# Kernel optimization log

Hardware: AMD Instinct MI355X
Metric: run time of the kernel (lower is better)

Reference implementation:

```python
import jax, jax.numpy as jnp
import numpy as np

N, E = 50000, 800000
IN_DIM, OUT_DIM, EDGE_DIM = 128, 128, 6
LN_EPS = 1e-5


def setup_inputs() -> dict:
    key = jax.random.key(0)
    ks = jax.random.split(key, 9)
    w = lambda k, sh: (jax.random.normal(k, sh, jnp.float32) * 0.05)
    return {
        "x": jax.random.normal(ks[0], (N, IN_DIM), jnp.float32),
        "edge_attr": jax.random.normal(ks[1], (E, EDGE_DIM), jnp.float32),
        "Wn": w(ks[2], (IN_DIM, OUT_DIM)),
        "bn": jnp.zeros((OUT_DIM,), jnp.float32),
        "We": w(ks[3], (EDGE_DIM, OUT_DIM)),
        "be": jnp.zeros((OUT_DIM,), jnp.float32),
        "Wm": w(ks[4], (2 * OUT_DIM, OUT_DIM)),
        "bm": jnp.zeros((OUT_DIM,), jnp.float32),
        "gamma": jnp.ones((OUT_DIM,), jnp.float32),
        "beta": jnp.zeros((OUT_DIM,), jnp.float32),
        "edge_index": jax.random.randint(ks[5], (2, E), 0, N, jnp.int32),
    }


def reference(x, edge_attr, Wn, bn, We, be, Wm, bm, gamma, beta, edge_index):
    row, col = edge_index[0], edge_index[1]
    x_t = x @ Wn + bn                                  # [N, D]
    e_t = edge_attr @ We + be                          # [E, D]
    msgs = jnp.concatenate([x_t[col], e_t], axis=-1)   # gather + concat [E, 2D]
    msgs = jax.nn.relu(msgs @ Wm + bm)                 # [E, D]
    agg = jax.ops.segment_sum(msgs, row, num_segments=N)            # scatter_add
    deg = jax.ops.segment_sum(jnp.ones((E,), jnp.float32), row, num_segments=N)
    out = agg / jnp.clip(deg, 1.0)[:, None] + x_t      # mean-normalize + residual
    mu = out.mean(axis=-1, keepdims=True)
    var = out.var(axis=-1, keepdims=True)
    return (out - mu) * jax.lax.rsqrt(var + LN_EPS) * gamma + beta
```

## Files before the change

### kernel.cpp

```cpp
#include <hip/hip_runtime.h>
#include <hip/hip_bf16.h>

#define D 128
#define EDGE_DIM 6
#define LN_EPS 1e-5f
#define HIST_BLOCKS 2048
#define BINE 2048
#define CB 256
#define NB2 196

typedef __attribute__((ext_vector_type(8))) short short8;
typedef __attribute__((ext_vector_type(4))) float f32x4;
typedef __attribute__((ext_vector_type(2))) float f32x2;

static __device__ __forceinline__ float bf_lo(unsigned u) { return __uint_as_float(u << 16); }
static __device__ __forceinline__ float bf_hi(unsigned u) { return __uint_as_float(u & 0xffff0000u); }
static __device__ __forceinline__ unsigned short f2bf(float f) {
    __hip_bfloat16 h = __float2bfloat16(f);
    return *reinterpret_cast<unsigned short*>(&h);
}
static __device__ __forceinline__ unsigned f2fp8(float f) {
    unsigned u;
    asm("v_cvt_pk_fp8_f32 %0, %1, %2" : "=v"(u) : "v"(f), "v"(0.0f));
    return u & 0xffu;
}
static __device__ __forceinline__ unsigned f2fp8pair(float a, float b) {
    unsigned u;
    asm("v_cvt_pk_fp8_f32 %0, %1, %2" : "=v"(u) : "v"(a), "v"(b));
    return u & 0xffffu;
}
static __device__ __forceinline__ f32x2 cvt2_fp8v(unsigned w) {
    f32x2 r;
    asm("v_cvt_pk_f32_fp8 %0, %1" : "=v"(r) : "v"(w));
    return r;
}
static __device__ __forceinline__ f32x2 cvt2_fp8s(unsigned w) {
    f32x2 r;
    asm("v_cvt_pk_f32_fp8 %0, %1" : "=v"(r) : "s"(w));
    return r;
}

__global__ __launch_bounds__(128)
void setup_all(const float* __restrict__ Wn, const float* __restrict__ bn,
               const float* __restrict__ We, const float* __restrict__ be,
               const float* __restrict__ Wm, const float* __restrict__ bm,
               const int* __restrict__ ei, int E,
               float* __restrict__ Wnm, float* __restrict__ bnm,
               float* __restrict__ Wc, float* __restrict__ bc,
               int* __restrict__ cnt) {
    const int b = blockIdx.x;
    const int d = threadIdx.x;
    if (b < 128) {
        float acc = 0.f;
#pragma unroll 8
        for (int j = 0; j < D; ++j)
            acc = fmaf(Wn[b * D + j], Wm[j * D + d], acc);
        Wnm[b * D + d] = acc;
    } else if (b == 128) {
        float acc = 0.f;
#pragma unroll 8
        for (int j = 0; j < D; ++j)
            acc = fmaf(bn[j], Wm[j * D + d], acc);
        bnm[d] = acc;
    } else if (b < 135) {
        const int k = b - 129;
        float acc = 0.f;
#pragma unroll 8
        for (int j = 0; j < D; ++j)
            acc = fmaf(We[k * D + j], Wm[(D + j) * D + d], acc);
        Wc[k * D + d] = acc;
    } else if (b == 135) {
        float acc = bm[d];
#pragma unroll 8
        for (int j = 0; j < D; ++j)
            acc = fmaf(be[j], Wm[(D + j) * D + d], acc);
        bc[d] = acc;
    } else {
        for (int i = (b - 136) * 128 + d; i < E; i += HIST_BLOCKS * 128)
            atomicAdd(&cnt[ei[i]], 1);
    }
}

__global__ __launch_bounds__(1024)
void scan_pack(const int* __restrict__ cnt, int* __restrict__ start,
               int* __restrict__ cur2, int* __restrict__ cursor, int n, int nscan,
               const float* __restrict__ Wn, const float* __restrict__ Wnm,
               unsigned short* __restrict__ Wb) {
    const int tid = threadIdx.x;
    if ((int)blockIdx.x >= nscan) {
        const int idx = ((int)blockIdx.x - nscan) * 1024 + tid;
        if (idx < 4096) {
            const int lane = idx & 63;
            const int s = (idx >> 6) & 3;
            const int ct = (idx >> 8) & 7;
            const int mat = idx >> 11;
            const float* W = mat ? Wnm : Wn;
            const int col = ct * 16 + (lane & 15);
            const int k0 = (lane >> 4) * 8 + 32 * s;
            short8 v;
#pragma unroll
            for (int j = 0; j < 8; ++j)
                v[j] = (short)f2bf(W[(size_t)(k0 + j) * D + col]);
            *reinterpret_cast<short8*>(Wb + (size_t)idx * 8) = v;
        }
        return;
    }
    __shared__ int wsum[16];
    __shared__ int sbase;
    const int lane = tid & 63, wid = tid >> 6;
    const int i = blockIdx.x * 1024 + tid;
    const int v = (i < n) ? cnt[i] : 0;
    int x = v;
#pragma unroll
    for (int off = 1; off < 64; off <<= 1) {
        int t = __shfl_up(x, off);
        if (lane >= off) x += t;
    }
    if (lane == 63) wsum[wid] = x;
    __syncthreads();
    if (wid == 0) {
        int w = (lane < 16) ? wsum[lane] : 0;
#pragma unroll
        for (int off = 1; off < 16; off <<= 1) {
            int t = __shfl_up(w, off);
            if (lane >= off) w += t;
        }
        if (lane < 16) wsum[lane] = w;
    }
    __syncthreads();
    const int total = wsum[15];
    if (tid == 0) sbase = atomicAdd(cursor, total);
    __syncthreads();
    const int woff = (wid > 0) ? wsum[wid - 1] : 0;
    if (i < n) {
        const int sv = sbase + woff + x - v;
        start[i] = sv;
        if ((i & (CB - 1)) == 0) cur2[i >> 8] = sv;
    }
}

__global__ __launch_bounds__(256)
void scat_gemm(const int* __restrict__ ei, int E, const float* __restrict__ ea,
               int* __restrict__ cur2, uint2* __restrict__ tmp,
               unsigned char* __restrict__ tmpR, int nbin,
               const float* __restrict__ x, const unsigned short* __restrict__ Wb,
               const float* __restrict__ bn, const float* __restrict__ bnm,
               unsigned short* __restrict__ xtb, unsigned char* __restrict__ hb,
               int nrows) {
    __shared__ unsigned short sP[BINE * 3];
    __shared__ int hist[NB2];
    __shared__ int cbase[NB2];
    const int tid = threadIdx.x;
    if ((int)blockIdx.x < nbin) {
        const int base = blockIdx.x * BINE;
        const int nrec = min(BINE, E - base);
        if (tid < NB2) hist[tid] = 0;
        const float2* ea2 = reinterpret_cast<const float2*>(ea);
        for (int i = tid; i < nrec * 3; i += 256) {
            float2 p = ea2[(size_t)base * 3 + i];
            sP[i] = (unsigned short)f2fp8pair(p.x, p.y);
        }
        int rows[8], cols[8];
#pragma unroll
        for (int it = 0; it < 8; ++it) {
            const int e = base + it * 256 + tid;
            const bool val = e < E;
            rows[it] = val ? ei[e] : -1;
            cols[it] = val ? ei[E + e] : 0;
        }
        __syncthreads();
#pragma unroll
        for (int it = 0; it < 8; ++it)
            if (rows[it] >= 0) atomicAdd(&hist[rows[it] >> 8], 1);
        __syncthreads();
        if (tid < NB2) {
            const int hv = hist[tid];
            cbase[tid] = hv ? atomicAdd(&cur2[tid], hv) : 0;
            hist[tid] = 0;
        }
        __syncthreads();
#pragma unroll
        for (int it = 0; it < 8; ++it)
            if (rows[it] >= 0) {
                const int bkt = rows[it] >> 8;
                const int lp = atomicAdd(&hist[bkt], 1);
                const int pos = cbase[bkt] + lp;
                const int le = (it * 256 + tid) * 3;
                const unsigned w0 = (unsigned)cols[it] | ((unsigned)sP[le] << 16);
                const unsigned w1 = (unsigned)sP[le + 1] | ((unsigned)sP[le + 2] << 16);
                tmp[pos] = make_uint2(w0, w1);
                tmpR[pos] = (unsigned char)(rows[it] & (CB - 1));
            }
        return;
    }
    const int ntile = (nrows + 15) / 16;
    const int lane = tid & 63;
    const int wid = tid >> 6;
    const int t = ((int)blockIdx.x - nbin) * 4 + wid;
    if (t >= ntile) return;
    const int row16 = lane & 15;
    const int kgrp = lane >> 4;

    float biasA[8], biasB[8];
#pragma unroll
    for (int ct = 0; ct < 8; ++ct) {
        biasA[ct] = bn[ct * 16 + row16];
        biasB[ct] = bnm[ct * 16 + row16];
    }
    const int ra = t * 16 + row16;
    const bool rv = ra < nrows;
    short8 a[4];
#pragma unroll
    for (int s = 0; s < 4; ++s) {
        const float* xp = x + (size_t)ra * D + kgrp * 8 + 32 * s;
        float4 u0 = rv ? *reinterpret_cast<const float4*>(xp)
                       : make_float4(0.f, 0.f, 0.f, 0.f);
        float4 u1 = rv ? *reinterpret_cast<const float4*>(xp + 4)
                       : make_float4(0.f, 0.f, 0.f, 0.f);
        a[s][0] = (short)f2bf(u0.x); a[s][1] = (short)f2bf(u0.y);
        a[s][2] = (short)f2bf(u0.z); a[s][3] = (short)f2bf(u0.w);
        a[s][4] = (short)f2bf(u1.x); a[s][5] = (short)f2bf(u1.y);
        a[s][6] = (short)f2bf(u1.z); a[s][7] = (short)f2bf(u1.w);
    }
    const int rw0 = t * 16 + kgrp * 4;
#pragma unroll
    for (int mat = 0; mat < 2; ++mat) {
#pragma unroll
        for (int ct = 0; ct < 8; ++ct) {
            f32x4 acc = {0.f, 0.f, 0.f, 0.f};
#pragma unroll
            for (int s = 0; s < 4; ++s) {
                short8 bfr = *reinterpret_cast<const short8*>(
                    Wb + (size_t)((((mat * 8 + ct) * 4 + s) * 64 + lane)) * 8);
                acc = __builtin_amdgcn_mfma_f32_16x16x32_bf16(a[s], bfr, acc, 0, 0, 0);
            }
            const float bsc = mat ? biasB[ct] : biasA[ct];
            const int dcol = ct * 16 + row16;
#pragma unroll
            for (int j = 0; j < 4; ++j) {
                const int r = rw0 + j;
                if (r < nrows) {
                    if (mat == 0)
                        xtb[(size_t)r * D + dcol] = f2bf(acc[j] + bsc);
                    else
                        hb[(size_t)r * D + dcol] = (unsigned char)f2fp8(acc[j] + bsc);
                }
            }
        }
    }
}

__global__ __launch_bounds__(512)
void resort(const uint2* __restrict__ tmp, const unsigned char* __restrict__ tmpR,
            const int* __restrict__ start, const int* __restrict__ cnt,
            uint2* __restrict__ rec, int nnode) {
    __shared__ uint2 sRec[2048];
    __shared__ unsigned char sRow[2048];
    __shared__ int ncur[CB];
    const int tid = threadIdx.x;
    const int b = blockIdx.x;
    const int nodes0 = b * CB;
    const int nn = min(CB, nnode - nodes0);
    if (tid < CB) ncur[tid] = (tid < nn) ? start[nodes0 + tid] : 0;
    __syncthreads();
    const int s0 = start[nodes0];
    const int lastn = nodes0 + nn - 1;
    const int count = start[lastn] + cnt[lastn] - s0;
    for (int base = 0; base < count; base += 2048) {
        const int m = min(2048, count - base);
        for (int i = tid; i < m; i += 512) {
            sRec[i] = tmp[(size_t)(s0 + base) + i];
            sRow[i] = tmpR[(size_t)(s0 + base) + i];
        }
        __syncthreads();
        for (int i = tid; i < m; i += 512) {
            const int rl = sRow[i];
            const int pos = atomicAdd(&ncur[rl], 1);
            rec[pos] = sRec[i];
        }
        __syncthreads();
    }
}

__global__ __launch_bounds__(256)
void aggregate_ln(const unsigned char* __restrict__ h8,
                  const int* __restrict__ start, const int* __restrict__ cnt,
                  const uint2* __restrict__ rec,
                  const float* __restrict__ Wc, const float* __restrict__ bc,
                  const unsigned* __restrict__ xtb,
                  const float* __restrict__ gamma, const float* __restrict__ beta,
                  float* __restrict__ out, int nnode) {
    const int lane = threadIdx.x & 63;
    const int wid = threadIdx.x >> 6;

    f32x2 wc[EDGE_DIM];
#pragma unroll
    for (int k = 0; k < EDGE_DIM; ++k)
        wc[k] = reinterpret_cast<const f32x2*>(Wc)[k * 64 + lane];
    const f32x2 bc2 = reinterpret_cast<const f32x2*>(bc)[lane];
    const f32x2 g = reinterpret_cast<const f32x2*>(gamma)[lane];
    const f32x2 bb = reinterpret_cast<const f32x2*>(beta)[lane];

    for (int n = blockIdx.x * 4 + wid; n < nnode; n += gridDim.x * 4) {
        const int s = start[n];
        const int c = cnt[n];
        const unsigned xu = xtb[(unsigned)(n * 64 + lane)];
        f32x2 axy = {0.f, 0.f};
        for (int ibase = 0; ibase < c; ibase += 64) {
            const int m = min(64, c - ibase);
            uint2 rc = make_uint2(0, 0);
            if (lane < m) rc = rec[(size_t)(s + ibase) + lane];
            auto LDH = [&](int j) -> unsigned {
                const int jc = min(j, m - 1);
                const unsigned colj =
                    (unsigned)__builtin_amdgcn_readlane((int)rc.x, jc) & 0xffffu;
                const unsigned short* hrow =
                    reinterpret_cast<const unsigned short*>(h8 + ((size_t)colj << 7));
                return hrow[lane];
            };
            auto COMP = [&](int j, unsigned hv) {
                const unsigned w0 = (unsigned)__builtin_amdgcn_readlane((int)rc.x, j);
                const unsigned w1 = (unsigned)__builtin_amdgcn_readlane((int)rc.y, j);
                const f32x2 e01 = cvt2_fp8s(w0 >> 16);
                const f32x2 e23 = cvt2_fp8s(w1 & 0xffffu);
                const f32x2 e45 = cvt2_fp8s(w1 >> 16);
                const f32x2 hx = cvt2_fp8v(hv);
                f32x2 mA, mB;
                asm("v_pk_add_f32 %0, %1, %2" : "=v"(mA) : "v"(bc2), "v"(hx));
                asm("v_pk_mul_f32 %0, %1, %2 op_sel:[1,0] op_sel_hi:[1,1]"
                    : "=v"(mB) : "v"(e01), "v"(wc[1]));
                asm("v_pk_fma_f32 %0, %1, %2, %0 op_sel:[0,0,0] op_sel_hi:[0,1,1]"
                    : "+v"(mA) : "v"(e01), "v"(wc[0]));
                asm("v_pk_fma_f32 %0, %1, %2, %0 op_sel:[1,0,0] op_sel_hi:[1,1,1]"
                    : "+v"(mB) : "v"(e23), "v"(wc[3]));
                asm("v_pk_fma_f32 %0, %1, %2, %0 op_sel:[0,0,0] op_sel_hi:[0,1,1]"
                    : "+v"(mA) : "v"(e23), "v"(wc[2]));
                asm("v_pk_fma_f32 %0, %1, %2, %0 op_sel:[1,0,0] op_sel_hi:[1,1,1]"
                    : "+v"(mB) : "v"(e45), "v"(wc[5]));
                asm("v_pk_fma_f32 %0, %1, %2, %0 op_sel:[0,0,0] op_sel_hi:[0,1,1]"
                    : "+v"(mA) : "v"(e45), "v"(wc[4]));
                asm("v_pk_add_f32 %0, %0, %1" : "+v"(mA) : "v"(mB));
                axy[0] += fmaxf(mA[0], 0.f);
                axy[1] += fmaxf(mA[1], 0.f);
            };
            unsigned h0 = LDH(0), h1 = LDH(1), h2 = LDH(2), h3 = LDH(3),
                     h4 = LDH(4), h5 = LDH(5), h6 = LDH(6), h7 = LDH(7);
            int i = 0;
            for (; i + 8 <= m; i += 8) {
                COMP(i + 0, h0); h0 = LDH(i + 8);
                COMP(i + 1, h1); h1 = LDH(i + 9);
                COMP(i + 2, h2); h2 = LDH(i + 10);
                COMP(i + 3, h3); h3 = LDH(i + 11);
                COMP(i + 4, h4); h4 = LDH(i + 12);
                COMP(i + 5, h5); h5 = LDH(i + 13);
                COMP(i + 6, h6); h6 = LDH(i + 14);
                COMP(i + 7, h7); h7 = LDH(i + 15);
            }
            if (i + 0 < m) COMP(i + 0, h0);
            if (i + 1 < m) COMP(i + 1, h1);
            if (i + 2 < m) COMP(i + 2, h2);
            if (i + 3 < m) COMP(i + 3, h3);
            if (i + 4 < m) COMP(i + 4, h4);
            if (i + 5 < m) COMP(i + 5, h5);
            if (i + 6 < m) COMP(i + 6, h6);
        }
        const float inv = 1.0f / fmaxf((float)c, 1.0f);
        float o0 = fmaf(axy[0], inv, bf_lo(xu));
        float o1 = fmaf(axy[1], inv, bf_hi(xu));
        float s1 = o0 + o1, s2 = o0 * o0 + o1 * o1;
#pragma unroll
        for (int off = 32; off; off >>= 1) {
            s1 += __shfl_xor(s1, off);
            s2 += __shfl_xor(s2, off);
        }
        const float mean = s1 * (1.0f / D);
        const float var = s2 * (1.0f / D) - mean * mean;
        const float rstd = rsqrtf(var + LN_EPS);
        float2 r;
        r.x = (o0 - mean) * rstd * g[0] + bb[0];
        r.y = (o1 - mean) * rstd * g[1] + bb[1];
        reinterpret_cast<float2*>(out)[(size_t)n * 64 + lane] = r;
    }
}

extern "C" void kernel_launch(void* const* d_in, const int* in_sizes, int n_in,
                              void* d_out, int out_size, void* d_ws, size_t ws_size,
                              hipStream_t stream) {
    const float* x     = (const float*)d_in[0];
    const float* eattr = (const float*)d_in[1];
    const float* Wn    = (const float*)d_in[2];
    const float* bn    = (const float*)d_in[3];
    const float* We    = (const float*)d_in[4];
    const float* be    = (const float*)d_in[5];
    const float* Wm    = (const float*)d_in[6];
    const float* bm    = (const float*)d_in[7];
    const float* gamma = (const float*)d_in[8];
    const float* beta  = (const float*)d_in[9];
    const int*   ei    = (const int*)d_in[10];

    const int N = in_sizes[0] / D;
    const int E = in_sizes[10] / 2;

    char* ws = (char*)d_ws;
    unsigned short* xtb = (unsigned short*)ws; ws += (size_t)N * D * 2;
    unsigned char*  hb  = (unsigned char*)ws;  ws += (size_t)N * D;
    int* ints = (int*)ws;                      ws += (size_t)(N + 4) * 4;
    int* cnt = ints;
    int* cursor = ints + N;
    int* cur2   = (int*)ws;                    ws += (size_t)(NB2 + 1) * 4;
    int* startv = (int*)ws;                    ws += (size_t)N * 4;
    uint2* rec  = (uint2*)ws;                  ws += (size_t)E * 8;
    float* Wnm  = (float*)ws;                  ws += (size_t)D * D * 4;
    float* bnm  = (float*)ws;                  ws += (size_t)D * 4;
    float* Wc   = (float*)ws;                  ws += (size_t)EDGE_DIM * D * 4;
    float* bcv  = (float*)ws;                  ws += (size_t)D * 4;
    unsigned short* Wb = (unsigned short*)ws;  ws += (size_t)4096 * 8 * 2;

    uint2* tmp = (uint2*)d_out;
    unsigned char* tmpR = (unsigned char*)d_out + (size_t)E * 8;

    const int nscan = (N + 1023) / 1024;
    const int nbin = (E + BINE - 1) / BINE;
    const int ntile = (N + 15) / 16;

    hipMemsetAsync(ints, 0, (size_t)(N + 4) * 4, stream);

    setup_all<<<136 + HIST_BLOCKS, 128, 0, stream>>>(Wn, bn, We, be, Wm, bm, ei, E,
                                                     Wnm, bnm, Wc, bcv, cnt);
    scan_pack<<<nscan + 4, 1024, 0, stream>>>(cnt, startv, cur2, cursor, N, nscan,
                                              Wn, Wnm, Wb);
    scat_gemm<<<nbin + (ntile + 3) / 4, 256, 0, stream>>>(ei, E, eattr, cur2, tmp, tmpR,
                                                          nbin, x, Wb, bn, bnm, xtb, hb, N);
    resort<<<NB2, 512, 0, stream>>>(tmp, tmpR, startv, cnt, rec, N);
    aggregate_ln<<<(N + 3) / 4, 256, 0, stream>>>(hb, startv, cnt, rec,
                                                  Wc, bcv, (const unsigned*)xtb,
                                                  gamma, beta, (float*)d_out, N);
}
```

Baseline: 149.8 us.

## Split wavefront into two half-waves each processing a different edge per step

The aggregation kernel now has each half of the 64-lane wavefront handle a different edge, with each lane covering four output features instead of two. Each lane loads a 4-byte fp8 row slice, so one gather instruction fetches two full 128-feature rows and the number of sequential edge iterations is halved. The halves are combined with a cross-half shuffle before the layernorm, and only the lower half writes the output as float4. The cost is more readlanes and selects per step, per-lane edge-feature conversions (vector instead of scalar), a masked accumulate for odd counts, and higher register pressure.

```diff
diff --git a/kernel.cpp b/kernel.cpp
--- a/kernel.cpp
+++ b/kernel.cpp
@@ -32,11 +32,6 @@
 static __device__ __forceinline__ f32x2 cvt2_fp8v(unsigned w) {
     f32x2 r;
     asm("v_cvt_pk_f32_fp8 %0, %1" : "=v"(r) : "v"(w));
-    return r;
-}
-static __device__ __forceinline__ f32x2 cvt2_fp8s(unsigned w) {
-    f32x2 r;
-    asm("v_cvt_pk_f32_fp8 %0, %1" : "=v"(r) : "s"(w));
     return r;
 }
 
@@ -292,94 +287,131 @@
                   float* __restrict__ out, int nnode) {
     const int lane = threadIdx.x & 63;
     const int wid = threadIdx.x >> 6;
-
-    f32x2 wc[EDGE_DIM];
-#pragma unroll
-    for (int k = 0; k < EDGE_DIM; ++k)
-        wc[k] = reinterpret_cast<const f32x2*>(Wc)[k * 64 + lane];
-    const f32x2 bc2 = reinterpret_cast<const f32x2*>(bc)[lane];
-    const f32x2 g = reinterpret_cast<const f32x2*>(gamma)[lane];
-    const f32x2 bb = reinterpret_cast<const f32x2*>(beta)[lane];
+    const int l5 = lane & 31;
+    const int half = lane >> 5;
+
+    f32x2 wcA[EDGE_DIM], wcB[EDGE_DIM];
+#pragma unroll
+    for (int k = 0; k < EDGE_DIM; ++k) {
+        wcA[k] = reinterpret_cast<const f32x2*>(Wc + k * D)[2 * l5];
+        wcB[k] = reinterpret_cast<const f32x2*>(Wc + k * D)[2 * l5 + 1];
+    }
+    const f32x2 bcA = reinterpret_cast<const f32x2*>(bc)[2 * l5];
+    const f32x2 bcB = reinterpret_cast<const f32x2*>(bc)[2 * l5 + 1];
 
     for (int n = blockIdx.x * 4 + wid; n < nnode; n += gridDim.x * 4) {
         const int s = start[n];
         const int c = cnt[n];
-        const unsigned xu = xtb[(unsigned)(n * 64 + lane)];
-        f32x2 axy = {0.f, 0.f};
+        f32x2 accA = {0.f, 0.f}, accB = {0.f, 0.f};
         for (int ibase = 0; ibase < c; ibase += 64) {
             const int m = min(64, c - ibase);
+            const int mq = (m + 1) >> 1;
             uint2 rc = make_uint2(0, 0);
             if (lane < m) rc = rec[(size_t)(s + ibase) + lane];
-            auto LDH = [&](int j) -> unsigned {
-                const int jc = min(j, m - 1);
-                const unsigned colj =
-                    (unsigned)__builtin_amdgcn_readlane((int)rc.x, jc) & 0xffffu;
-                const unsigned short* hrow =
-                    reinterpret_cast<const unsigned short*>(h8 + ((size_t)colj << 7));
-                return hrow[lane];
+            auto LDP = [&](int t) -> unsigned {
+                const int jA = 2 * t;
+                const int jB = min(2 * t + 1, m - 1);
+                const unsigned cA = (unsigned)__builtin_amdgcn_readlane((int)rc.x, jA) & 0xffffu;
+                const unsigned cB = (unsigned)__builtin_amdgcn_readlane((int)rc.x, jB) & 0xffffu;
+                const unsigned col = half ? cB : cA;
+                return *reinterpret_cast<const unsigned*>(
+                    h8 + ((size_t)col << 7) + 4 * l5);
             };
-            auto COMP = [&](int j, unsigned hv) {
-                const unsigned w0 = (unsigned)__builtin_amdgcn_readlane((int)rc.x, j);
-                const unsigned w1 = (unsigned)__builtin_amdgcn_readlane((int)rc.y, j);
-                const f32x2 e01 = cvt2_fp8s(w0 >> 16);
-                const f32x2 e23 = cvt2_fp8s(w1 & 0xffffu);
-                const f32x2 e45 = cvt2_fp8s(w1 >> 16);
-                const f32x2 hx = cvt2_fp8v(hv);
-                f32x2 mA, mB;
-                asm("v_pk_add_f32 %0, %1, %2" : "=v"(mA) : "v"(bc2), "v"(hx));
+            auto PCOMP = [&](int t, unsigned hv) {
+                const int jA = 2 * t;
+                const int jBr = min(2 * t + 1, m - 1);
+                const unsigned w0A = (unsigned)__builtin_amdgcn_readlane((int)rc.x, jA);
+                const unsigned w0B = (unsigned)__builtin_amdgcn_readlane((int)rc.x, jBr);
+                const unsigned w1A = (unsigned)__builtin_amdgcn_readlane((int)rc.y, jA);
+                const unsigned w1B = (unsigned)__builtin_amdgcn_readlane((int)rc.y, jBr);
+                const unsigned w0 = half ? w0B : w0A;
+                const unsigned w1 = half ? w1B : w1A;
+                const f32x2 e01 = cvt2_fp8v(w0 >> 16);
+                const f32x2 e23 = cvt2_fp8v(w1 & 0xffffu);
+                const f32x2 e45 = cvt2_fp8v(w1 >> 16);
+                const f32x2 h01 = cvt2_fp8v(hv);
+                const f32x2 h23 = cvt2_fp8v(hv >> 16);
+                f32x2 mA, mB, nA, nB;
+                asm("v_pk_add_f32 %0, %1, %2" : "=v"(mA) : "v"(bcA), "v"(h01));
+                asm("v_pk_add_f32 %0, %1, %2" : "=v"(nA) : "v"(bcB), "v"(h23));
                 asm("v_pk_mul_f32 %0, %1, %2 op_sel:[1,0] op_sel_hi:[1,1]"
-                    : "=v"(mB) : "v"(e01), "v"(wc[1]));
-                asm("v_pk_fma_f32 %0, %1, %2, %0 op_sel:[0,0,0] op_sel_hi:[0,1,1]"
-                    : "+v"(mA) : "v"(e01), "v"(wc[0]));
+                    : "=v"(mB) : "v"(e01), "v"(wcA[1]));
+                asm("v_pk_mul_f32 %0, %1, %2 op_sel:[1,0] op_sel_hi:[1,1]"
+                    : "=v"(nB) : "v"(e01), "v"(wcB[1]));
+                asm("v_pk_fma_f32 %0, %1, %2, %0 op_sel:[0,0,0] op_sel_hi:[0,1,1]"
+                    : "+v"(mA) : "v"(e01), "v"(wcA[0]));
+                asm("v_pk_fma_f32 %0, %1, %2, %0 op_sel:[0,0,0] op_sel_hi:[0,1,1]"
+                    : "+v"(nA) : "v"(e01), "v"(wcB[0]));
                 asm("v_pk_fma_f32 %0, %1, %2, %0 op_sel:[1,0,0] op_sel_hi:[1,1,1]"
-                    : "+v"(mB) : "v"(e23), "v"(wc[3]));
-                asm("v_pk_fma_f32 %0, %1, %2, %0 op_sel:[0,0,0] op_sel_hi:[0,1,1]"
-                    : "+v"(mA) : "v"(e23), "v"(wc[2]));
+                    : "+v"(mB) : "v"(e23), "v"(wcA[3]));
                 asm("v_pk_fma_f32 %0, %1, %2, %0 op_sel:[1,0,0] op_sel_hi:[1,1,1]"
-                    : "+v"(mB) : "v"(e45), "v"(wc[5]));
-                asm("v_pk_fma_f32 %0, %1, %2, %0 op_sel:[0,0,0] op_sel_hi:[0,1,1]"
-                    : "+v"(mA) : "v"(e45), "v"(wc[4]));
+                    : "+v"(nB) : "v"(e23), "v"(wcB[3]));
+                asm("v_pk_fma_f32 %0, %1, %2, %0 op_sel:[0,0,0] op_sel_hi:[0,1,1]"
+                    : "+v"(mA) : "v"(e23), "v"(wcA[2]));
+                asm("v_pk_fma_f32 %0, %1, %2, %0 op_sel:[0,0,0] op_sel_hi:[0,1,1]"
+                    : "+v"(nA) : "v"(e23), "v"(wcB[2]));
+                asm("v_pk_fma_f32 %0, %1, %2, %0 op_sel:[1,0,0] op_sel_hi:[1,1,1]"
+                    : "+v"(mB) : "v"(e45), "v"(wcA[5]));
+                asm("v_pk_fma_f32 %0, %1, %2, %0 op_sel:[1,0,0] op_sel_hi:[1,1,1]"
+                    : "+v"(nB) : "v"(e45), "v"(wcB[5]));
+                asm("v_pk_fma_f32 %0, %1, %2, %0 op_sel:[0,0,0] op_sel_hi:[0,1,1]"
+                    : "+v"(mA) : "v"(e45), "v"(wcA[4]));
+                asm("v_pk_fma_f32 %0, %1, %2, %0 op_sel:[0,0,0] op_sel_hi:[0,1,1]"
+                    : "+v"(nA) : "v"(e45), "v"(wcB[4]));
                 asm("v_pk_add_f32 %0, %0, %1" : "+v"(mA) : "v"(mB));
-                axy[0] += fmaxf(mA[0], 0.f);
-                axy[1] += fmaxf(mA[1], 0.f);
+                asm("v_pk_add_f32 %0, %0, %1" : "+v"(nA) : "v"(nB));
+                const float keep = (half == 0 || 2 * t + 1 < m) ? 1.0f : 0.0f;
+                accA[0] = fmaf(keep, fmaxf(mA[0], 0.f), accA[0]);
+                accA[1] = fmaf(keep, fmaxf(mA[1], 0.f), accA[1]);
+                accB[0] = fmaf(keep, fmaxf(nA[0], 0.f), accB[0]);
+                accB[1] = fmaf(keep, fmaxf(nA[1], 0.f), accB[1]);
             };
-            unsigned h0 = LDH(0), h1 = LDH(1), h2 = LDH(2), h3 = LDH(3),
-                     h4 = LDH(4), h5 = LDH(5), h6 = LDH(6), h7 = LDH(7);
-            int i = 0;
-            for (; i + 8 <= m; i += 8) {
-                COMP(i + 0, h0); h0 = LDH(i + 8);
-                COMP(i + 1, h1); h1 = LDH(i + 9);
-                COMP(i + 2, h2); h2 = LDH(i + 10);
-                COMP(i + 3, h3); h3 = LDH(i + 11);
-                COMP(i + 4, h4); h4 = LDH(i + 12);
-                COMP(i + 5, h5); h5 = LDH(i + 13);
-                COMP(i + 6, h6); h6 = LDH(i + 14);
-                COMP(i + 7, h7); h7 = LDH(i + 15);
+            unsigned h0 = LDP(0), h1 = 0, h2 = 0, h3 = 0;
+            if (1 < mq) h1 = LDP(1);
+            if (2 < mq) h2 = LDP(2);
+            if (3 < mq) h3 = LDP(3);
+            for (int q = 0; q < 32; q += 4) {
+                if (q >= mq) break;
+                { PCOMP(q + 0, h0); if (q + 4 < mq) h0 = LDP(q + 4); }
+                if (q + 1 < mq) { PCOMP(q + 1, h1); if (q + 5 < mq) h1 = LDP(q + 5); }
+                if (q + 2 < mq) { PCOMP(q + 2, h2); if (q + 6 < mq) h2 = LDP(q + 6); }
+                if (q + 3 < mq) { PCOMP(q + 3, h3); if (q + 7 < mq) h3 = LDP(q + 7); }
             }
-            if (i + 0 < m) COMP(i + 0, h0);
-            if (i + 1 < m) COMP(i + 1, h1);
-            if (i + 2 < m) COMP(i + 2, h2);
-            if (i + 3 < m) COMP(i + 3, h3);
-            if (i + 4 < m) COMP(i + 4, h4);
-            if (i + 5 < m) COMP(i + 5, h5);
-            if (i + 6 < m) COMP(i + 6, h6);
-        }
+        }
+        accA[0] += __shfl_xor(accA[0], 32);
+        accA[1] += __shfl_xor(accA[1], 32);
+        accB[0] += __shfl_xor(accB[0], 32);
+        accB[1] += __shfl_xor(accB[1], 32);
+
         const float inv = 1.0f / fmaxf((float)c, 1.0f);
-        float o0 = fmaf(axy[0], inv, bf_lo(xu));
-        float o1 = fmaf(axy[1], inv, bf_hi(xu));
-        float s1 = o0 + o1, s2 = o0 * o0 + o1 * o1;
-#pragma unroll
-        for (int off = 32; off; off >>= 1) {
+        const uint2 xq = reinterpret_cast<const uint2*>(xtb)[(size_t)n * 32 + l5];
+        float o[4];
+        o[0] = fmaf(accA[0], inv, bf_lo(xq.x));
+        o[1] = fmaf(accA[1], inv, bf_hi(xq.x));
+        o[2] = fmaf(accB[0], inv, bf_lo(xq.y));
+        o[3] = fmaf(accB[1], inv, bf_hi(xq.y));
+        float s1 = o[0] + o[1] + o[2] + o[3];
+        float s2 = o[0] * o[0] + o[1] * o[1] + o[2] * o[2] + o[3] * o[3];
+#pragma unroll
+        for (int off = 1; off <= 16; off <<= 1) {
             s1 += __shfl_xor(s1, off);
             s2 += __shfl_xor(s2, off);
         }
         const float mean = s1 * (1.0f / D);
         const float var = s2 * (1.0f / D) - mean * mean;
         const float rstd = rsqrtf(var + LN_EPS);
-        float2 r;
-        r.x = (o0 - mean) * rstd * g[0] + bb[0];
-        r.y = (o1 - mean) * rstd * g[1] + bb[1];
-        reinterpret_cast<float2*>(out)[(size_t)n * 64 + lane] = r;
+        if (half == 0) {
+            const f32x2 gA = reinterpret_cast<const f32x2*>(gamma)[2 * l5];
+            const f32x2 gB = reinterpret_cast<const f32x2*>(gamma)[2 * l5 + 1];
+            const f32x2 bA = reinterpret_cast<const f32x2*>(beta)[2 * l5];
+            const f32x2 bB = reinterpret_cast<const f32x2*>(beta)[2 * l5 + 1];
+            float4 r;
+            r.x = (o[0] - mean) * rstd * gA[0] + bA[0];
+            r.y = (o[1] - mean) * rstd * gA[1] + bA[1];
+            r.z = (o[2] - mean) * rstd * gB[0] + bB[0];
+            r.w = (o[3] - mean) * rstd * gB[1] + bB[1];
+            reinterpret_cast<float4*>(out)[(size_t)n * 32 + l5] = r;
+        }
     }
 }
 
```

Result: slower. 156.4 us (+4.4%).

## Stage bucketed edge records in shared memory before coalesced global scatter

Applied to the files above, without the earlier changes.

Each binning block first computes a local exclusive prefix over the bucket histogram and writes every edge record into shared memory grouped by bucket. It then copies the grouped records to their global positions in linear order. The aim is to replace random per-edge global writes with mostly contiguous writes. In exchange it uses more LDS (about 28 KB extra), adds a block-wide scan with many barriers, and needs a second shared counter array.

```diff
diff --git a/kernel.cpp b/kernel.cpp
--- a/kernel.cpp
+++ b/kernel.cpp
@@ -148,13 +148,19 @@
                unsigned short* __restrict__ xtb, unsigned char* __restrict__ hb,
                int nrows) {
     __shared__ unsigned short sP[BINE * 3];
-    __shared__ int hist[NB2];
+    __shared__ uint2 sRec[BINE];
+    __shared__ unsigned char sBkt[BINE];
+    __shared__ unsigned char sRowOut[BINE];
+    __shared__ int hist[256];
+    __shared__ int incl[256];
+    __shared__ int hist2[NB2];
     __shared__ int cbase[NB2];
     const int tid = threadIdx.x;
     if ((int)blockIdx.x < nbin) {
         const int base = blockIdx.x * BINE;
         const int nrec = min(BINE, E - base);
-        if (tid < NB2) hist[tid] = 0;
+        hist[tid] = 0;
+        if (tid < NB2) hist2[tid] = 0;
         const float2* ea2 = reinterpret_cast<const float2*>(ea);
         for (int i = tid; i < nrec * 3; i += 256) {
             float2 p = ea2[(size_t)base * 3 + i];
@@ -176,21 +182,38 @@
         if (tid < NB2) {
             const int hv = hist[tid];
             cbase[tid] = hv ? atomicAdd(&cur2[tid], hv) : 0;
-            hist[tid] = 0;
-        }
-        __syncthreads();
+        }
+        const int myv = hist[tid];
+        incl[tid] = myv;
+        __syncthreads();
+#pragma unroll
+        for (int off = 1; off < 256; off <<= 1) {
+            const int t = (tid >= off) ? incl[tid - off] : 0;
+            __syncthreads();
+            incl[tid] += t;
+            __syncthreads();
+        }
 #pragma unroll
         for (int it = 0; it < 8; ++it)
             if (rows[it] >= 0) {
                 const int bkt = rows[it] >> 8;
-                const int lp = atomicAdd(&hist[bkt], 1);
-                const int pos = cbase[bkt] + lp;
+                const int lst = incl[bkt] - hist[bkt];
+                const int ls = lst + atomicAdd(&hist2[bkt], 1);
                 const int le = (it * 256 + tid) * 3;
                 const unsigned w0 = (unsigned)cols[it] | ((unsigned)sP[le] << 16);
                 const unsigned w1 = (unsigned)sP[le + 1] | ((unsigned)sP[le + 2] << 16);
-                tmp[pos] = make_uint2(w0, w1);
-                tmpR[pos] = (unsigned char)(rows[it] & (CB - 1));
+                sRec[ls] = make_uint2(w0, w1);
+                sBkt[ls] = (unsigned char)bkt;
+                sRowOut[ls] = (unsigned char)(rows[it] & (CB - 1));
             }
+        __syncthreads();
+        const int total = incl[255];
+        for (int i = tid; i < total; i += 256) {
+            const int b = sBkt[i];
+            const int g = cbase[b] + (i - (incl[b] - hist[b]));
+            tmp[g] = sRec[i];
+            tmpR[g] = sRowOut[i];
+        }
         return;
     }
     const int ntile = (nrows + 15) / 16;
```

Measured after the change: 150.1 us. No clear change (+0.2%).
